# Kernel optimization log

Measured on AMD Instinct MI355X. Metric: run time of the kernel, lower is better.

The kernel has to match this reference:

```python
import jax, jax.numpy as jnp
import numpy as np

HIDDEN = 2048
NUM_HEADS = 16
Q_LORA = 1536
KV_LORA = 512
QK_NOPE = 128
QK_ROPE = 64
V_HEAD = 128
EPS = 1e-6
QK_HEAD = QK_NOPE + QK_ROPE  # 192


def rmsnorm(x, w, eps=EPS):
    xf = x.astype(jnp.float32)
    var = jnp.mean(xf * xf, axis=-1, keepdims=True)
    return (w * (xf * jax.lax.rsqrt(var + eps)).astype(x.dtype))


def setup_inputs() -> dict:
    key = jax.random.key(0)
    ks = jax.random.split(key, 8)
    B, S = 1, 2048
    hidden_states = jax.random.normal(ks[0], (B, S, HIDDEN), dtype=jnp.float32)
    # causal additive mask [B,1,S,S]
    causal = jnp.tril(jnp.ones((S, S), dtype=bool))
    attention_mask = jnp.where(causal, 0.0, -1e9).astype(jnp.float32)[None, None]
    s = lambda fan_in: 1.0 / np.sqrt(fan_in)
    Wqa = jax.random.normal(ks[1], (HIDDEN, Q_LORA), dtype=jnp.float32) * s(HIDDEN)
    gqa = jnp.ones((Q_LORA,), dtype=jnp.float32)
    Wqb = jax.random.normal(ks[2], (Q_LORA, NUM_HEADS * QK_HEAD), dtype=jnp.float32) * s(Q_LORA)
    Wkva = jax.random.normal(ks[3], (HIDDEN, KV_LORA + QK_ROPE), dtype=jnp.float32) * s(HIDDEN)
    gkva = jnp.ones((KV_LORA,), dtype=jnp.float32)
    Wkvb = jax.random.normal(ks[4], (KV_LORA, NUM_HEADS * (QK_NOPE + V_HEAD)), dtype=jnp.float32) * s(KV_LORA)
    Wo = jax.random.normal(ks[5], (NUM_HEADS * V_HEAD, HIDDEN), dtype=jnp.float32) * s(NUM_HEADS * V_HEAD)
    return {"hidden_states": hidden_states, "attention_mask": attention_mask,
            "Wqa": Wqa, "gqa": gqa, "Wqb": Wqb, "Wkva": Wkva, "gkva": gkva,
            "Wkvb": Wkvb, "Wo": Wo}


def reference(hidden_states, attention_mask, Wqa, gqa, Wqb, Wkva, gkva, Wkvb, Wo):
    B, S, _ = hidden_states.shape
    # Q path: low-rank down-proj + RMSNorm + up-proj
    q_c = rmsnorm(hidden_states @ Wqa, gqa)
    q = (q_c @ Wqb).reshape(B, S, NUM_HEADS, QK_HEAD).transpose(0, 2, 1, 3)  # [B,H,S,192]
    # KV path: joint down-proj, split latent and shared rope part
    kv_c = hidden_states @ Wkva  # [B,S,KV_LORA+ROPE]
    kv_a, k_rope = kv_c[..., :KV_LORA], kv_c[..., KV_LORA:]
    kv = (rmsnorm(kv_a, gkva) @ Wkvb).reshape(B, S, NUM_HEADS, QK_NOPE + V_HEAD)
    k_nope, v = kv[..., :QK_NOPE], kv[..., QK_NOPE:]
    # shared rope part broadcast across heads (no rotary actually applied in source)
    k_rope_b = jnp.broadcast_to(k_rope[:, :, None, :], (B, S, NUM_HEADS, QK_ROPE))
    k = jnp.concatenate([k_nope, k_rope_b], axis=-1).transpose(0, 2, 1, 3)  # [B,H,S,192]
    v = v.transpose(0, 2, 1, 3)  # [B,H,S,128]
    scale = 1.0 / np.sqrt(QK_HEAD)
    attn = jnp.einsum("bhqd,bhkd->bhqk", q, k) * scale
    attn = attn + attention_mask
    attn = jax.nn.softmax(attn.astype(jnp.float32), axis=-1).astype(v.dtype)
    out = jnp.einsum("bhqk,bhkd->bhqd", attn, v)  # [B,H,S,128]
    out = out.transpose(0, 2, 1, 3).reshape(B, S, NUM_HEADS * V_HEAD)
    return out @ Wo
```

## Files before the change

kernel.cpp:

```cpp
#include <hip/hip_runtime.h>
#include <hip/hip_bf16.h>

typedef __bf16 bf16;
typedef __bf16 bf16x8 __attribute__((ext_vector_type(8)));
typedef __bf16 bf16x4 __attribute__((ext_vector_type(4)));
typedef float f32x4 __attribute__((ext_vector_type(4)));

#define HIDDEN 2048
#define SEQ 2048
#define NH 16
#define QL 1536
#define KVL 512
#define SCALE_LOG2E 0.10411754631f

__device__ __forceinline__ void gload_lds16(const void* g, void* l) {
  typedef const __attribute__((address_space(1))) void* gp_t;
  typedef __attribute__((address_space(3))) void* lp_t;
  __builtin_amdgcn_global_load_lds((gp_t)(unsigned long long)g,
                                   (lp_t)(unsigned int)(unsigned long long)l, 16, 0, 0);
}

__device__ __forceinline__ float fexp2(float x) {
  float r; asm("v_exp_f32 %0, %1" : "=v"(r) : "v"(x)); return r;
}
__device__ __forceinline__ unsigned cvt_pk_bf16(float lo, float hi) {
  unsigned r; asm("v_cvt_pk_bf16_f32 %0, %1, %2" : "=v"(r) : "v"(lo), "v"(hi)); return r;
}

__global__ void k_prep(const float* __restrict__ hidden, bf16* __restrict__ Xb,
                       const float* __restrict__ Wqa, bf16* __restrict__ WqaT,
                       const float* __restrict__ Wqb, bf16* __restrict__ WqbT,
                       const float* __restrict__ Wkva, bf16* __restrict__ WkvaT,
                       const float* __restrict__ Wkvb, bf16* __restrict__ WkvbT,
                       const float* __restrict__ Wo, bf16* __restrict__ WoT) {
  __shared__ float tile[32][33];
  int b = blockIdx.x, tid = threadIdx.x;
  const float* W; bf16* Wt; int K, N, bx, by;
  if (b < 3072)       { W = Wqa;  Wt = WqaT;  K = 2048; N = 1536; int r = b;         bx = r % 48;  by = r / 48; }
  else if (b < 7680)  { W = Wqb;  Wt = WqbT;  K = 1536; N = 3072; int r = b - 3072;  bx = r % 96;  by = r / 96; }
  else if (b < 8832)  { W = Wkva; Wt = WkvaT; K = 2048; N = 576;  int r = b - 7680;  bx = r % 18;  by = r / 18; }
  else if (b < 10880) { W = Wkvb; Wt = WkvbT; K = 512;  N = 4096; int r = b - 8832;  bx = r % 128; by = r / 128; }
  else if (b < 14976) { W = Wo;   Wt = WoT;   K = 2048; N = 2048; int r = b - 10880; bx = r % 64;  by = r / 64; }
  else {
    int r = b - 14976;
    int base = (r * 256 + tid) * 4;
    float4 v = *(const float4*)(hidden + base);
    bf16x4 o = { (bf16)v.x, (bf16)v.y, (bf16)v.z, (bf16)v.w };
    *(bf16x4*)(Xb + base) = o;
    return;
  }
  int n0 = bx * 32, k0 = by * 32, cc = tid & 31, rr = tid >> 5;
#pragma unroll
  for (int it = 0; it < 4; ++it) {
    int r = it * 8 + rr;
    tile[r][cc] = W[(size_t)(k0 + r) * N + n0 + cc];
  }
  __syncthreads();
#pragma unroll
  for (int it = 0; it < 4; ++it) {
    int r = it * 8 + rr;
    Wt[(size_t)(n0 + r) * K + k0 + cc] = (bf16)tile[cc][r];
  }
}

__device__ __forceinline__ void gemm_body(const bf16* __restrict__ A, const bf16* __restrict__ Bt,
                                          bf16* __restrict__ Cb, float* __restrict__ Cf,
                                          int N, int Kfull, int kbase, int Klen,
                                          int m0, int n0, bf16* As, bf16* Bs) {
  int tid = threadIdx.x, lane = tid & 63, w = tid >> 6;
  int wr = w >> 1, wc = w & 1;
  int l15 = lane & 15, l4 = lane >> 4;
  f32x4 acc[4][4] = {};
  for (int k0 = kbase; k0 < kbase + Klen; k0 += 64) {
#pragma unroll
    for (int i = 0; i < 4; ++i) {
      int c = w * 4 + i;
      int row = c * 8 + (lane >> 3);
      int col = (lane & 7) * 8;
      gload_lds16(&A[(size_t)(m0 + row) * Kfull + k0 + col], &As[c * 512]);
      gload_lds16(&Bt[(size_t)(n0 + row) * Kfull + k0 + col], &Bs[c * 512]);
    }
    __syncthreads();
#pragma unroll
    for (int kk = 0; kk < 2; ++kk) {
      bf16x8 af[4], bfr[4];
#pragma unroll
      for (int m = 0; m < 4; ++m)
        af[m] = *(const bf16x8*)&As[(wr * 64 + m * 16 + l15) * 64 + kk * 32 + l4 * 8];
#pragma unroll
      for (int n = 0; n < 4; ++n)
        bfr[n] = *(const bf16x8*)&Bs[(wc * 64 + n * 16 + l15) * 64 + kk * 32 + l4 * 8];
      __builtin_amdgcn_s_setprio(1);
#pragma unroll
      for (int m = 0; m < 4; ++m)
#pragma unroll
        for (int n = 0; n < 4; ++n)
          acc[m][n] = __builtin_amdgcn_mfma_f32_16x16x32_bf16(af[m], bfr[n], acc[m][n], 0, 0, 0);
      __builtin_amdgcn_s_setprio(0);
    }
    __syncthreads();
  }
#pragma unroll
  for (int m = 0; m < 4; ++m)
#pragma unroll
    for (int n = 0; n < 4; ++n)
#pragma unroll
      for (int r = 0; r < 4; ++r) {
        int grow = m0 + wr * 64 + m * 16 + l4 * 4 + r;
        int gcol = n0 + wc * 64 + n * 16 + l15;
        if (gcol < N) {
          float v = acc[m][n][r];
          if (Cf) Cf[(size_t)grow * N + gcol] = v;
          else Cb[(size_t)grow * N + gcol] = (bf16)v;
        }
      }
}

__global__ __launch_bounds__(256) void k_gemm_a(const bf16* __restrict__ Xb,
                                                const bf16* __restrict__ B1, const bf16* __restrict__ B2,
                                                float* __restrict__ qa0, float* __restrict__ qa1,
                                                float* __restrict__ kvc0, float* __restrict__ kvc1) {
  __shared__ __align__(16) bf16 As[128 * 64];
  __shared__ __align__(16) bf16 Bs[128 * 64];
  int by = blockIdx.y;
  if (by < 24) {
    int yy = by >> 1, kh = by & 1;
    gemm_body(Xb, B1, nullptr, kh ? qa1 : qa0, 1536, 2048, kh * 1024, 1024,
              blockIdx.x * 128, yy * 128, As, Bs);
  } else {
    int r = by - 24, yy = r >> 1, kh = r & 1;
    gemm_body(Xb, B2, nullptr, kh ? kvc1 : kvc0, 576, 2048, kh * 1024, 1024,
              blockIdx.x * 128, yy * 128, As, Bs);
  }
}

__global__ __launch_bounds__(256) void k_gemm_b(const bf16* __restrict__ A1, const bf16* __restrict__ A2,
                                                const bf16* __restrict__ B1, const bf16* __restrict__ B2,
                                                bf16* __restrict__ C1, bf16* __restrict__ C2) {
  __shared__ __align__(16) bf16 As[128 * 64];
  __shared__ __align__(16) bf16 Bs[128 * 64];
  int by = blockIdx.y;
  if (by < 24) gemm_body(A1, B1, C1, nullptr, 3072, 1536, 0, 1536, blockIdx.x * 128, by * 128, As, Bs);
  else         gemm_body(A2, B2, C2, nullptr, 4096, 512, 0, 512, blockIdx.x * 128, (by - 24) * 128, As, Bs);
}

__global__ __launch_bounds__(256) void k_gemm_sk(const bf16* __restrict__ A, const bf16* __restrict__ Bt,
                                                 float* __restrict__ O0, float* __restrict__ O1) {
  __shared__ __align__(16) bf16 As[128 * 64];
  __shared__ __align__(16) bf16 Bs[128 * 64];
  int by = blockIdx.y, nt = by >> 1, kh = by & 1;
  gemm_body(A, Bt, nullptr, kh ? O1 : O0, 2048, 2048, kh * 1024, 1024,
            blockIdx.x * 128, nt * 128, As, Bs);
}

__global__ void k_add(const float* __restrict__ O0, const float* __restrict__ O1,
                      float* __restrict__ out) {
  int base = (blockIdx.x * 256 + threadIdx.x) * 4;
  float4 a = *(const float4*)(O0 + base);
  float4 b = *(const float4*)(O1 + base);
  float4 o = { a.x + b.x, a.y + b.y, a.z + b.z, a.w + b.w };
  *(float4*)(out + base) = o;
}

__device__ inline float block_reduce_sum(float v, float* red) {
#pragma unroll
  for (int off = 1; off < 64; off <<= 1) v += __shfl_xor(v, off);
  int w = threadIdx.x >> 6;
  if ((threadIdx.x & 63) == 0) red[w] = v;
  __syncthreads();
  return red[0] + red[1] + red[2] + red[3];
}

__global__ void k_rms_all(const float* __restrict__ qa0, const float* __restrict__ qa1,
                          const float* __restrict__ gq, bf16* __restrict__ qc,
                          const float* __restrict__ kvc0, const float* __restrict__ kvc1,
                          const float* __restrict__ gkv,
                          bf16* __restrict__ kvn, bf16* __restrict__ kr) {
  __shared__ float red[4];
  int b = blockIdx.x, tid = threadIdx.x;
  if (b < 2048) {
    int row = b;
    float v[6];
    float ss = 0.f;
#pragma unroll
    for (int j = 0; j < 6; ++j) {
      size_t idx = (size_t)row * QL + tid + j * 256;
      v[j] = qa0[idx] + qa1[idx];
      ss += v[j] * v[j];
    }
    float tot = block_reduce_sum(ss, red);
    float rs = rsqrtf(tot / (float)QL + 1e-6f);
#pragma unroll
    for (int j = 0; j < 6; ++j) {
      int c = tid + j * 256;
      qc[(size_t)row * QL + c] = (bf16)(v[j] * rs * gq[c]);
    }
  } else {
    int row = b - 2048;
    size_t base = (size_t)row * 576;
    float v0 = kvc0[base + tid] + kvc1[base + tid];
    float v1 = kvc0[base + tid + 256] + kvc1[base + tid + 256];
    float tot = block_reduce_sum(v0 * v0 + v1 * v1, red);
    float rs = rsqrtf(tot / (float)KVL + 1e-6f);
    kvn[(size_t)row * KVL + tid] = (bf16)(v0 * rs * gkv[tid]);
    kvn[(size_t)row * KVL + tid + 256] = (bf16)(v1 * rs * gkv[tid + 256]);
    if (tid < 64) kr[row * 64 + tid] = (bf16)(kvc0[base + 512 + tid] + kvc1[base + 512 + tid]);
  }
}

__global__ void k_vt(const bf16* __restrict__ KVm, bf16* __restrict__ VT) {
  __shared__ bf16 tile[32][34];
  int b = blockIdx.x, tid = threadIdx.x;
  int h = b >> 8, rem = b & 255;
  int d0 = (rem >> 6) * 32, s0 = (rem & 63) * 32;
  int cc = tid & 31, rr = tid >> 5;
#pragma unroll
  for (int it = 0; it < 4; ++it) {
    int r = it * 8 + rr;
    tile[r][cc] = KVm[(size_t)(s0 + r) * 4096 + h * 256 + 128 + d0 + cc];
  }
  __syncthreads();
#pragma unroll
  for (int it = 0; it < 4; ++it) {
    int r = it * 8 + rr;
    VT[((size_t)(h * 128 + d0 + r)) * 2048 + s0 + cc] = tile[cc][r];
  }
}

__global__ __launch_bounds__(256) void k_attn(const bf16* __restrict__ Q, const bf16* __restrict__ KV,
                                              const bf16* __restrict__ KR, const bf16* __restrict__ VT,
                                              bf16* __restrict__ O) {
  __shared__ __align__(16) bf16 Ks[64 * 192];
  __shared__ __align__(16) bf16 Vt[128 * 64];
  __shared__ __align__(16) bf16 Ps[4 * 16 * 64];
  int bid = blockIdx.x;
  int h = bid & 15, i = bid >> 4;
  int qb = (i < 16) ? i : 47 - i;
  int q0 = qb * 64;
  int tid = threadIdx.x, lane = tid & 63, w = tid >> 6;
  int l15 = lane & 15, l4 = lane >> 4;
  int sw = (l15 & 7) << 4;
  char* PTw = (char*)Ps + w * 2048;
  const bf16* VTh = VT + (size_t)h * 128 * 2048;

  bf16x8 aq[6];
  int qrow = q0 + w * 16 + l15;
#pragma unroll
  for (int ks = 0; ks < 6; ++ks)
    aq[ks] = *(const bf16x8*)&Q[(size_t)qrow * 3072 + h * 192 + ks * 32 + l4 * 8];

  f32x4 oacc[8] = {};
  float mrun = -1e30f, lrun = 0.f;
  int nt = qb + 1;
  for (int t = 0; t < nt; ++t) {
#pragma unroll
    for (int it = 0; it < 6; ++it) {
      int idx = it * 256 + tid;
      int r = idx / 24, gg = idx - r * 24;
      int c = gg ^ (r & 7);
      const bf16* src = (c < 16) ? &KV[(size_t)(t * 64 + r) * 4096 + h * 256 + c * 8]
                                 : &KR[(size_t)(t * 64 + r) * 64 + (c - 16) * 8];
      gload_lds16(src, (char*)Ks + (it * 256 + w * 64) * 16);
    }
#pragma unroll
    for (int it = 0; it < 4; ++it) {
      int idx = it * 256 + tid;
      int d = idx >> 3, cc = idx & 7, c = cc ^ (d & 7);
      gload_lds16(&VTh[(size_t)d * 2048 + t * 64 + c * 8], (char*)Vt + (it * 256 + w * 64) * 16);
    }
    __syncthreads();

    f32x4 sacc[4] = {};
    __builtin_amdgcn_s_setprio(1);
#pragma unroll
    for (int ks = 0; ks < 6; ++ks) {
      int co = (((ks << 2) + l4) << 4) ^ sw;
#pragma unroll
      for (int n = 0; n < 4; ++n) {
        bf16x8 ak = *(const bf16x8*)((char*)Ks + (n * 16 + l15) * 384 + co);
        sacc[n] = __builtin_amdgcn_mfma_f32_16x16x32_bf16(ak, aq[ks], sacc[n], 0, 0, 0);
      }
    }
    __builtin_amdgcn_s_setprio(0);

    bool maskt = (t == qb);
#pragma unroll
    for (int n = 0; n < 4; ++n)
#pragma unroll
      for (int r = 0; r < 4; ++r) {
        float v = sacc[n][r] * SCALE_LOG2E;
        if (maskt) {
          int kvp = t * 64 + n * 16 + l4 * 4 + r;
          if (kvp > qrow) v = -1e30f;
        }
        sacc[n][r] = v;
      }

    float mx = sacc[0][0];
#pragma unroll
    for (int n = 0; n < 4; ++n)
#pragma unroll
      for (int r = 0; r < 4; ++r) mx = fmaxf(mx, sacc[n][r]);
    mx = fmaxf(mx, __shfl_xor(mx, 16));
    mx = fmaxf(mx, __shfl_xor(mx, 32));
    if (__any(mx - mrun > 8.0f)) {
      float mn = fmaxf(mrun, mx);
      float al = fexp2(mrun - mn);
      mrun = mn;
      lrun *= al;
#pragma unroll
      for (int vf = 0; vf < 8; ++vf) oacc[vf] *= al;
    }
    float rsum = 0.f;
#pragma unroll
    for (int n = 0; n < 4; ++n) {
      float e0 = fexp2(sacc[n][0] - mrun);
      float e1 = fexp2(sacc[n][1] - mrun);
      float e2 = fexp2(sacc[n][2] - mrun);
      float e3 = fexp2(sacc[n][3] - mrun);
      rsum += (e0 + e1) + (e2 + e3);
      uint2 u;
      u.x = cvt_pk_bf16(e0, e1);
      u.y = cvt_pk_bf16(e2, e3);
      *(uint2*)(PTw + l15 * 128 + ((n * 32 + l4 * 8) ^ sw)) = u;
    }
    rsum += __shfl_xor(rsum, 16);
    rsum += __shfl_xor(rsum, 32);
    lrun += rsum;

    __builtin_amdgcn_s_setprio(1);
#pragma unroll
    for (int ks = 0; ks < 2; ++ks) {
      int co = (((ks << 2) + l4) << 4) ^ sw;
      bf16x8 ap = *(const bf16x8*)(PTw + l15 * 128 + co);
#pragma unroll
      for (int vf = 0; vf < 8; ++vf) {
        bf16x8 av = *(const bf16x8*)((char*)Vt + (vf * 16 + l15) * 128 + co);
        oacc[vf] = __builtin_amdgcn_mfma_f32_16x16x32_bf16(av, ap, oacc[vf], 0, 0, 0);
      }
    }
    __builtin_amdgcn_s_setprio(0);
    __syncthreads();
  }

  char* OTw = (char*)Ks + w * 4096;
  float inv = 1.0f / lrun;
#pragma unroll
  for (int vf = 0; vf < 8; ++vf) {
    unsigned ua = cvt_pk_bf16(oacc[vf][0] * inv, oacc[vf][1] * inv);
    unsigned ub = cvt_pk_bf16(oacc[vf][2] * inv, oacc[vf][3] * inv);
    int base = vf * 32 + l4 * 8;
    *(unsigned*)(OTw + l15 * 256 + ((base + 0) ^ sw)) = ua;
    *(unsigned*)(OTw + l15 * 256 + ((base + 4) ^ sw)) = ub;
  }
  int qq = lane >> 2, c0 = lane & 3;
  size_t obase = (size_t)(q0 + w * 16 + qq) * 2048 + h * 128;
#pragma unroll
  for (int ii = 0; ii < 4; ++ii) {
    int ck = ii * 4 + c0;
    bf16x8 v = *(const bf16x8*)(OTw + qq * 256 + ((ck * 16) ^ ((qq & 7) << 4)));
    *(bf16x8*)&O[obase + ck * 8] = v;
  }
}

extern "C" void kernel_launch(void* const* d_in, const int* in_sizes, int n_in,
                              void* d_out, int out_size, void* d_ws, size_t ws_size,
                              hipStream_t stream) {
  (void)in_sizes; (void)n_in; (void)out_size; (void)ws_size;
  const float* hidden = (const float*)d_in[0];
  const float* Wqa  = (const float*)d_in[2];
  const float* gqa  = (const float*)d_in[3];
  const float* Wqb  = (const float*)d_in[4];
  const float* Wkva = (const float*)d_in[5];
  const float* gkva = (const float*)d_in[6];
  const float* Wkvb = (const float*)d_in[7];
  const float* Wo   = (const float*)d_in[8];
  float* out = (float*)d_out;

  char* ws = (char*)d_ws;
  size_t off = 0;
  auto alloc = [&](size_t bytes) {
    char* p = ws + off;
    off += (bytes + 255) & ~(size_t)255;
    return p;
  };
  bf16* Xb     = (bf16*)alloc((size_t)SEQ * HIDDEN * 2);
  bf16* WqaT   = (bf16*)alloc((size_t)QL * HIDDEN * 2);
  bf16* WqbT   = (bf16*)alloc((size_t)3072 * QL * 2);
  bf16* WkvaT  = (bf16*)alloc((size_t)576 * HIDDEN * 2);
  bf16* WkvbT  = (bf16*)alloc((size_t)4096 * KVL * 2);
  bf16* WoT    = (bf16*)alloc((size_t)2048 * 2048 * 2);
  float* qa0   = (float*)alloc((size_t)SEQ * QL * 4);
  float* qa1   = (float*)alloc((size_t)SEQ * QL * 4);
  float* kvc0  = (float*)alloc((size_t)SEQ * 576 * 4);
  float* kvc1  = (float*)alloc((size_t)SEQ * 576 * 4);
  bf16* qc     = (bf16*)alloc((size_t)SEQ * QL * 2);
  bf16* kvn    = (bf16*)alloc((size_t)SEQ * KVL * 2);
  bf16* krope  = (bf16*)alloc((size_t)SEQ * 64 * 2);
  bf16* Qm     = (bf16*)alloc((size_t)SEQ * 3072 * 2);
  bf16* KVm    = (bf16*)alloc((size_t)SEQ * 4096 * 2);
  bf16* VTg    = (bf16*)alloc((size_t)NH * 128 * SEQ * 2);
  bf16* Om     = (bf16*)alloc((size_t)SEQ * 2048 * 2);
  float* O0 = qa0;
  float* O1 = (float*)KVm;

  k_prep<<<19072, 256, 0, stream>>>(hidden, Xb, Wqa, WqaT, Wqb, WqbT,
                                    Wkva, WkvaT, Wkvb, WkvbT, Wo, WoT);
  k_gemm_a<<<dim3(16, 34), 256, 0, stream>>>(Xb, WqaT, WkvaT, qa0, qa1, kvc0, kvc1);
  k_rms_all<<<4096, 256, 0, stream>>>(qa0, qa1, gqa, qc, kvc0, kvc1, gkva, kvn, krope);
  k_gemm_b<<<dim3(16, 56), 256, 0, stream>>>(qc, kvn, WqbT, WkvbT, Qm, KVm);
  k_vt<<<4096, 256, 0, stream>>>(KVm, VTg);
  k_attn<<<512, 256, 0, stream>>>(Qm, KVm, krope, VTg, Om);
  k_gemm_sk<<<dim3(16, 32), 256, 0, stream>>>(Om, WoT, O0, O1);
  k_add<<<4096, 256, 0, stream>>>(O0, O1, out);
}
```

Baseline: 228.7 us.

## Double-buffer K/V tiles in attention and pass P through lane shuffles

The attention kernel now keeps two LDS buffers for the K and V^T tiles and issues the next tile's async global-to-LDS loads before computing on the current one, waiting on a partial vmcnt so memory latency overlaps with MFMA work. It also drops the per-wave P scratch in LDS and rebuilds the MFMA operand for P from register values with cross-lane shuffles. The cost is roughly double the K/V LDS footprint, which may lower occupancy, plus extra shuffle instructions. Correctness depends on the hand-set vmcnt count matching the number of outstanding loads.

```diff
diff --git a/kernel.cpp b/kernel.cpp
--- a/kernel.cpp
+++ b/kernel.cpp
@@ -230,9 +230,8 @@
 __global__ __launch_bounds__(256) void k_attn(const bf16* __restrict__ Q, const bf16* __restrict__ KV,
                                               const bf16* __restrict__ KR, const bf16* __restrict__ VT,
                                               bf16* __restrict__ O) {
-  __shared__ __align__(16) bf16 Ks[64 * 192];
-  __shared__ __align__(16) bf16 Vt[128 * 64];
-  __shared__ __align__(16) bf16 Ps[4 * 16 * 64];
+  __shared__ __align__(16) bf16 KsD[2][64 * 192];
+  __shared__ __align__(16) bf16 VtD[2][128 * 64];
   int bid = blockIdx.x;
   int h = bid & 15, i = bid >> 4;
   int qb = (i < 16) ? i : 47 - i;
@@ -240,7 +239,6 @@
   int tid = threadIdx.x, lane = tid & 63, w = tid >> 6;
   int l15 = lane & 15, l4 = lane >> 4;
   int sw = (l15 & 7) << 4;
-  char* PTw = (char*)Ps + w * 2048;
   const bf16* VTh = VT + (size_t)h * 128 * 2048;
 
   bf16x8 aq[6];
@@ -252,7 +250,10 @@
   f32x4 oacc[8] = {};
   float mrun = -1e30f, lrun = 0.f;
   int nt = qb + 1;
-  for (int t = 0; t < nt; ++t) {
+
+  auto STAGE = [&](int buf, int t) {
+    char* kb = (char*)KsD[buf];
+    char* vb = (char*)VtD[buf];
 #pragma unroll
     for (int it = 0; it < 6; ++it) {
       int idx = it * 256 + tid;
@@ -260,15 +261,29 @@
       int c = gg ^ (r & 7);
       const bf16* src = (c < 16) ? &KV[(size_t)(t * 64 + r) * 4096 + h * 256 + c * 8]
                                  : &KR[(size_t)(t * 64 + r) * 64 + (c - 16) * 8];
-      gload_lds16(src, (char*)Ks + (it * 256 + w * 64) * 16);
+      gload_lds16(src, kb + (it * 256 + w * 64) * 16);
     }
 #pragma unroll
     for (int it = 0; it < 4; ++it) {
       int idx = it * 256 + tid;
-      int d = idx >> 3, cc = idx & 7, c = cc ^ (d & 7);
-      gload_lds16(&VTh[(size_t)d * 2048 + t * 64 + c * 8], (char*)Vt + (it * 256 + w * 64) * 16);
-    }
-    __syncthreads();
+      int d = idx >> 3, c2 = idx & 7, c = c2 ^ (d & 7);
+      gload_lds16(&VTh[(size_t)d * 2048 + t * 64 + c * 8], vb + (it * 256 + w * 64) * 16);
+    }
+  };
+
+  STAGE(0, 0);
+  for (int t = 0; t < nt; ++t) {
+    int cur = t & 1;
+    if (t + 1 < nt) {
+      STAGE(cur ^ 1, t + 1);
+      asm volatile("s_waitcnt vmcnt(10)" ::: "memory");
+    } else {
+      asm volatile("s_waitcnt vmcnt(0)" ::: "memory");
+    }
+    __builtin_amdgcn_s_barrier();
+    __builtin_amdgcn_sched_barrier(0);
+    const char* Kb = (const char*)KsD[cur];
+    const char* Vb = (const char*)VtD[cur];
 
     f32x4 sacc[4] = {};
     __builtin_amdgcn_s_setprio(1);
@@ -277,7 +292,7 @@
       int co = (((ks << 2) + l4) << 4) ^ sw;
 #pragma unroll
       for (int n = 0; n < 4; ++n) {
-        bf16x8 ak = *(const bf16x8*)((char*)Ks + (n * 16 + l15) * 384 + co);
+        bf16x8 ak = *(const bf16x8*)(Kb + (n * 16 + l15) * 384 + co);
         sacc[n] = __builtin_amdgcn_mfma_f32_16x16x32_bf16(ak, aq[ks], sacc[n], 0, 0, 0);
       }
     }
@@ -312,6 +327,7 @@
       for (int vf = 0; vf < 8; ++vf) oacc[vf] *= al;
     }
     float rsum = 0.f;
+    unsigned pk[4][2];
 #pragma unroll
     for (int n = 0; n < 4; ++n) {
       float e0 = fexp2(sacc[n][0] - mrun);
@@ -319,31 +335,45 @@
       float e2 = fexp2(sacc[n][2] - mrun);
       float e3 = fexp2(sacc[n][3] - mrun);
       rsum += (e0 + e1) + (e2 + e3);
-      uint2 u;
-      u.x = cvt_pk_bf16(e0, e1);
-      u.y = cvt_pk_bf16(e2, e3);
-      *(uint2*)(PTw + l15 * 128 + ((n * 32 + l4 * 8) ^ sw)) = u;
+      pk[n][0] = cvt_pk_bf16(e0, e1);
+      pk[n][1] = cvt_pk_bf16(e2, e3);
     }
     rsum += __shfl_xor(rsum, 16);
     rsum += __shfl_xor(rsum, 32);
     lrun += rsum;
 
+    int srcA = l15 + ((l4 & 1) << 5);
+    int srcB = srcA + 16;
+    int sel = l4 >> 1;
     __builtin_amdgcn_s_setprio(1);
 #pragma unroll
     for (int ks = 0; ks < 2; ++ks) {
+      unsigned a00 = (unsigned)__shfl((int)pk[2 * ks][0], srcA);
+      unsigned a10 = (unsigned)__shfl((int)pk[2 * ks + 1][0], srcA);
+      unsigned a01 = (unsigned)__shfl((int)pk[2 * ks][1], srcA);
+      unsigned a11 = (unsigned)__shfl((int)pk[2 * ks + 1][1], srcA);
+      unsigned b00 = (unsigned)__shfl((int)pk[2 * ks][0], srcB);
+      unsigned b10 = (unsigned)__shfl((int)pk[2 * ks + 1][0], srcB);
+      unsigned b01 = (unsigned)__shfl((int)pk[2 * ks][1], srcB);
+      unsigned b11 = (unsigned)__shfl((int)pk[2 * ks + 1][1], srcB);
+      union { unsigned u[4]; bf16x8 v; } ap;
+      ap.u[0] = sel ? a10 : a00;
+      ap.u[1] = sel ? a11 : a01;
+      ap.u[2] = sel ? b10 : b00;
+      ap.u[3] = sel ? b11 : b01;
       int co = (((ks << 2) + l4) << 4) ^ sw;
-      bf16x8 ap = *(const bf16x8*)(PTw + l15 * 128 + co);
 #pragma unroll
       for (int vf = 0; vf < 8; ++vf) {
-        bf16x8 av = *(const bf16x8*)((char*)Vt + (vf * 16 + l15) * 128 + co);
-        oacc[vf] = __builtin_amdgcn_mfma_f32_16x16x32_bf16(av, ap, oacc[vf], 0, 0, 0);
+        bf16x8 av = *(const bf16x8*)(Vb + (vf * 16 + l15) * 128 + co);
+        oacc[vf] = __builtin_amdgcn_mfma_f32_16x16x32_bf16(av, ap.v, oacc[vf], 0, 0, 0);
       }
     }
     __builtin_amdgcn_s_setprio(0);
-    __syncthreads();
-  }
-
-  char* OTw = (char*)Ks + w * 4096;
+    __builtin_amdgcn_s_barrier();
+  }
+
+  int curF = (nt - 1) & 1;
+  char* OTw = (char*)KsD[curF] + w * 4096;
   float inv = 1.0f / lrun;
 #pragma unroll
   for (int vf = 0; vf < 8; ++vf) {
```

After: 219.7 us. -4.0%, faster.
